# Kernel tuning notes

Hardware: AMD Instinct MI355X
Metric: run time of the kernel (lower is better)

## Reference

```python
import jax, jax.numpy as jnp
import numpy as np


def setup_inputs() -> dict:
    key = jax.random.key(0)
    ks = jax.random.split(key, 7)
    B, D, d1, d2, d3 = 256, 256, 1024, 512, 256
    s = lambda f: 1.0 / np.sqrt(f)  # torch nn.Linear-style init scale
    return {
        "x": jax.random.normal(ks[0], (B, D), jnp.float32),
        "W1": jax.random.normal(ks[1], (d1, D), jnp.float32) * s(D),
        "b1": jax.random.normal(ks[2], (d1,), jnp.float32) * s(D),
        "W2": jax.random.normal(ks[3], (d2, d1), jnp.float32) * s(d1),
        "b2": jax.random.normal(ks[4], (d2,), jnp.float32) * s(d1),
        "W3": jax.random.normal(ks[5], (d3, d2), jnp.float32) * s(d2),
        "b3": jax.random.normal(ks[6], (d3,), jnp.float32) * s(d2),
        "k": 10,
    }


def _border_dists(x, W1, b1, W2, b2, W3, b3):
    # Layer 1: pre-activations and boundary distances. For the first layer the
    # effective linear map is W1 itself (shared across the batch).
    z1 = x @ W1.T + b1                                   # [B, d1]
    dist1 = jnp.abs(z1) / jnp.linalg.norm(W1, axis=1)    # [B, d1]
    m1 = (z1 > 0).astype(x.dtype)
    V1 = m1[:, :, None] * W1[None]                       # [B, d1, D] per-instance map after ReLU
    h1 = m1 * z1

    # Layer 2
    z2 = h1 @ W2.T + b2                                  # [B, d2]
    V2 = jnp.einsum('oi,bid->bod', W2, V1)               # [B, d2, D]
    dist2 = jnp.abs(z2) / jnp.linalg.norm(V2, axis=2)
    m2 = (z2 > 0).astype(x.dtype)
    h2 = m2 * z2

    # Layer 3
    z3 = h2 @ W3.T + b3                                  # [B, d3]
    V3 = jnp.einsum('oi,bid->bod', W3, m2[:, :, None] * V2)  # [B, d3, D]
    dist3 = jnp.abs(z3) / jnp.linalg.norm(V3, axis=2)

    return jnp.concatenate([dist1, dist2, dist3], axis=1)  # [B, d1+d2+d3]


def reference(x, W1, b1, W2, b2, W3, b3, k):
    dists = _border_dists(x, W1, b1, W2, b2, W3, b3)
    # smallest-k distances per instance via top_k on negated distances
    neg_top, _ = jax.lax.top_k(-dists, k)                # [B, k]
    return jnp.sum(-neg_top)                             # border-distance loss (scalar)
```

## Files before the change

kernel.cpp:

```cpp
#include <hip/hip_runtime.h>
#include <math.h>
#include <float.h>

#define B   256
#define D   256
#define D1  1024
#define D2  512
#define D3  256
#define NDIST (D1 + D2 + D3)
#define CQ  2.0f

typedef __attribute__((ext_vector_type(8))) short short8;
typedef __attribute__((ext_vector_type(4))) float f32x4;
typedef __attribute__((ext_vector_type(4))) int   i32x4;

__device__ __forceinline__ float waveReduceSum(float v) {
    #pragma unroll
    for (int off = 32; off > 0; off >>= 1)
        v += __shfl_down(v, off, 64);
    return v;
}
__device__ __forceinline__ float waveReduceMax(float v) {
    #pragma unroll
    for (int off = 32; off > 0; off >>= 1)
        v = fmaxf(v, __shfl_down(v, off, 64));
    return v;
}
__device__ __forceinline__ unsigned short f2bf(float f) {
    unsigned int u = __float_as_uint(f);
    u = (u + 0x7FFFu + ((u >> 16) & 1u)) >> 16;
    return (unsigned short)u;
}
__device__ __forceinline__ float bf2f(unsigned short h) {
    return __uint_as_float(((unsigned int)h) << 16);
}
__device__ __forceinline__ void gld16(const void* g, void* l) {
    __builtin_amdgcn_global_load_lds(
        (const __attribute__((address_space(1))) unsigned int*)g,
        (__attribute__((address_space(3))) unsigned int*)l, 16, 0, 0);
}
__device__ __forceinline__ int swz_src(int row, int lane) {
    return ((lane & 3) + ((row >> 1) & 3)) & 3;
}
__device__ __forceinline__ int swz_frag(int row, int quad) {
    return row * 32 + (((quad - ((row >> 1) & 3)) & 3) * 8);
}

__global__ __launch_bounds__(256) void k_prep(
    const float* __restrict__ x,  const float* __restrict__ W1,
    const float* __restrict__ W2, const float* __restrict__ W3,
    float* __restrict__ zeros,
    float* __restrict__ outp,
    unsigned short* __restrict__ xhi,  unsigned short* __restrict__ xlo,
    unsigned short* __restrict__ W1hi, unsigned short* __restrict__ W1lo,
    unsigned short* __restrict__ W2hi, unsigned short* __restrict__ W2lo,
    unsigned short* __restrict__ W3hi, unsigned short* __restrict__ W3lo,
    signed char* __restrict__ W1Ti8, float* __restrict__ saq,
    signed char* __restrict__ W2i8,  float* __restrict__ sbq,
    signed char* __restrict__ W3i8,  float* __restrict__ s3q,
    float* __restrict__ rn1) {
    int blk = blockIdx.x;
    int t = threadIdx.x;
    if (blk < 1536) {
        if (blk == 0 && t == 0) outp[0] = 0.f;
        zeros[blk * 256 + t] = 0.f;
        return;
    }
    if (blk < 2496) {
        int i4 = ((blk - 1536) * 256 + t) * 4;
        const float* src; unsigned short *hi, *lo; int off;
        if (i4 < 65536)       { src = x;  hi = xhi;  lo = xlo;  off = i4; }
        else if (i4 < 327680) { src = W1; hi = W1hi; lo = W1lo; off = i4 - 65536; }
        else if (i4 < 851968) { src = W2; hi = W2hi; lo = W2lo; off = i4 - 327680; }
        else                  { src = W3; hi = W3hi; lo = W3lo; off = i4 - 851968; }
        float4 v = *(const float4*)(src + off);
        ushort4 h, l;
        h.x = f2bf(v.x); l.x = f2bf(v.x - bf2f(h.x));
        h.y = f2bf(v.y); l.y = f2bf(v.y - bf2f(h.y));
        h.z = f2bf(v.z); l.z = f2bf(v.z - bf2f(h.z));
        h.w = f2bf(v.w); l.w = f2bf(v.w - bf2f(h.w));
        *(ushort4*)(hi + off) = h;
        *(ushort4*)(lo + off) = l;
        return;
    }
    if (blk < 2528) {
        int ty = t >> 5, tx = t & 31;
        int d = (blk - 2496) * 8 + ty;
        float m = 0.f;
        for (int i = tx; i < D1; i += 32) m = fmaxf(m, fabsf(W1[(size_t)i * D + d]));
        #pragma unroll
        for (int off = 16; off > 0; off >>= 1) m = fmaxf(m, __shfl_down(m, off, 32));
        m = __shfl(m, 0, 32);
        m = fmaxf(m, 1e-20f);
        if (tx == 0) saq[d] = m / 127.f;
        float inv = 127.f / m;
        for (int i = tx; i < D1; i += 32) {
            int q = __float2int_rn(W1[(size_t)i * D + d] * inv);
            W1Ti8[(size_t)d * D1 + i] = (signed char)q;
        }
        return;
    }
    if (blk < 2656) {
        int o = (blk - 2528) * 4 + (t >> 6);
        int l = t & 63;
        const float* row = W2 + (size_t)o * D1;
        float m = 0.f;
        for (int tt = l; tt < D1; tt += 64) m = fmaxf(m, fabsf(row[tt]));
        m = waveReduceMax(m);
        m = __shfl(m, 0, 64);
        m = fmaxf(m, 1e-20f);
        if (l == 0) sbq[o] = m / 127.f;
        float inv = 127.f / m;
        for (int tt = l; tt < D1; tt += 64)
            W2i8[(size_t)o * D1 + tt] = (signed char)__float2int_rn(row[tt] * inv);
        return;
    }
    if (blk < 2720) {
        int p = (blk - 2656) * 4 + (t >> 6);
        int l = t & 63;
        const float* row = W3 + (size_t)p * D2;
        float m = 0.f;
        for (int tt = l; tt < D2; tt += 64) m = fmaxf(m, fabsf(row[tt]));
        m = waveReduceMax(m);
        m = __shfl(m, 0, 64);
        m = fmaxf(m, 1e-20f);
        if (l == 0) s3q[p] = m / 127.f;
        float inv = 127.f / m;
        for (int tt = l; tt < D2; tt += 64)
            W3i8[(size_t)p * D2 + tt] = (signed char)__float2int_rn(row[tt] * inv);
        return;
    }
    {
        int gw = (blk - 2720) * 4 + (t >> 6);
        int lane = t & 63;
        const float* row = W1 + (size_t)gw * D;
        float s = 0.f;
        for (int tt = lane; tt < D; tt += 64) { float v = row[tt]; s += v * v; }
        s = waveReduceSum(s);
        if (lane == 0) rn1[gw] = sqrtf(s);
    }
}

template <int KD, int KL>
__device__ __forceinline__ void mfma3_64(
    const unsigned short* __restrict__ Ahi, const unsigned short* __restrict__ Alo,
    const unsigned short* __restrict__ Bhi, const unsigned short* __restrict__ Blo,
    int m0, int n0, int k0, unsigned short* sm, f32x4 acc[2][2]) {
    int tid = threadIdx.x;
    int l = tid & 63, w = tid >> 6;
    int rsub = l >> 2;
    int quad = l >> 4, l16 = l & 15;
    int wm = (w >> 1) * 32, wn = (w & 1) * 32;
    unsigned short* sAh = sm;
    unsigned short* sAl = sm + 2048;
    unsigned short* sBh = sm + 4096;
    unsigned short* sBl = sm + 6144;
    ptrdiff_t dA = Alo - Ahi, dB = Blo - Bhi;
    int rloc = w * 16 + rsub;
    int c = swz_src(rloc, l);
    const unsigned short* pa = Ahi + (size_t)(m0 + rloc) * KD + k0 + c * 8;
    const unsigned short* pb = Bhi + (size_t)(n0 + rloc) * KD + k0 + c * 8;
    int aoff[2], boff[2];
    #pragma unroll
    for (int mt = 0; mt < 2; mt++) aoff[mt] = swz_frag(wm + mt * 16 + l16, quad);
    #pragma unroll
    for (int nt = 0; nt < 2; nt++) boff[nt] = swz_frag(wn + nt * 16 + l16, quad);
    for (int kk = 0; kk < KL; kk += 32) {
        gld16(pa + kk,      sAh + w * 512);
        gld16(pa + dA + kk, sAl + w * 512);
        gld16(pb + kk,      sBh + w * 512);
        gld16(pb + dB + kk, sBl + w * 512);
        __syncthreads();
        short8 ah[2], al[2], bh[2], bl[2];
        #pragma unroll
        for (int mt = 0; mt < 2; mt++) {
            ah[mt] = *(const short8*)(sAh + aoff[mt]);
            al[mt] = *(const short8*)(sAl + aoff[mt]);
        }
        #pragma unroll
        for (int nt = 0; nt < 2; nt++) {
            bh[nt] = *(const short8*)(sBh + boff[nt]);
            bl[nt] = *(const short8*)(sBl + boff[nt]);
        }
        #pragma unroll
        for (int mt = 0; mt < 2; mt++)
            #pragma unroll
            for (int nt = 0; nt < 2; nt++) {
                acc[mt][nt] = __builtin_amdgcn_mfma_f32_16x16x32_bf16(ah[mt], bh[nt], acc[mt][nt], 0, 0, 0);
                acc[mt][nt] = __builtin_amdgcn_mfma_f32_16x16x32_bf16(ah[mt], bl[nt], acc[mt][nt], 0, 0, 0);
                acc[mt][nt] = __builtin_amdgcn_mfma_f32_16x16x32_bf16(al[mt], bh[nt], acc[mt][nt], 0, 0, 0);
            }
        __syncthreads();
    }
}

__global__ __launch_bounds__(256) void k_l1(
    const unsigned short* __restrict__ xhi,  const unsigned short* __restrict__ xlo,
    const unsigned short* __restrict__ W1hi, const unsigned short* __restrict__ W1lo,
    const float* __restrict__ b1, const float* __restrict__ rn1,
    float* __restrict__ dists, unsigned char* __restrict__ m1q,
    unsigned short* __restrict__ h1hi, unsigned short* __restrict__ h1lo) {
    __shared__ __align__(16) unsigned short sm[8192];
    int m0 = blockIdx.x * 64, n0 = blockIdx.y * 64;
    f32x4 acc[2][2] = {};
    mfma3_64<D, D>(xhi, xlo, W1hi, W1lo, m0, n0, 0, sm, acc);
    int l = threadIdx.x & 63, w = threadIdx.x >> 6;
    int quad = l >> 4, l16 = l & 15;
    int wm = (w >> 1) * 32, wn = (w & 1) * 32;
    #pragma unroll
    for (int mt = 0; mt < 2; mt++)
        #pragma unroll
        for (int nt = 0; nt < 2; nt++) {
            int n = n0 + wn + nt * 16 + l16;
            float bv = b1[n], rv = rn1[n];
            #pragma unroll
            for (int r = 0; r < 4; r++) {
                int m = m0 + wm + mt * 16 + quad * 4 + r;
                float z = acc[mt][nt][r] + bv;
                size_t idx = (size_t)m * D1 + n;
                dists[idx] = fabsf(z) / rv;
                m1q[idx] = (z > 0.f) ? 0xFFu : 0u;
                float h = z > 0.f ? z : 0.f;
                unsigned short hh = f2bf(h);
                h1hi[idx] = hh;
                h1lo[idx] = f2bf(h - bf2f(hh));
            }
        }
}

__global__ __launch_bounds__(256) void k_big1(
    const unsigned short* __restrict__ h1hi, const unsigned short* __restrict__ h1lo,
    const unsigned short* __restrict__ W2hi, const unsigned short* __restrict__ W2lo,
    float* __restrict__ z2,
    const signed char* __restrict__ W1Ti8,
    const signed char* __restrict__ W2i8,
    const unsigned char* __restrict__ m1q,
    const float* __restrict__ saq,
    const float* __restrict__ sbq,
    signed char* __restrict__ qV2,
    float* __restrict__ norm2) {
    __shared__ __align__(16) unsigned char smem[32768];
    int bid = blockIdx.x;

    if (bid < 128) {
        unsigned short* sm = (unsigned short*)smem;
        int m0 = (bid & 3) * 64, n0 = ((bid >> 2) & 7) * 64, k0 = (bid >> 5) * 256;
        f32x4 acc[2][2] = {};
        mfma3_64<D1, 256>(h1hi, h1lo, W2hi, W2lo, m0, n0, k0, sm, acc);
        int l = threadIdx.x & 63, w = threadIdx.x >> 6;
        int quad = l >> 4, l16 = l & 15;
        int wm = (w >> 1) * 32, wn = (w & 1) * 32;
        #pragma unroll
        for (int mt = 0; mt < 2; mt++)
            #pragma unroll
            for (int nt = 0; nt < 2; nt++) {
                int n = n0 + wn + nt * 16 + l16;
                #pragma unroll
                for (int r = 0; r < 4; r++) {
                    int m = m0 + wm + mt * 16 + quad * 4 + r;
                    atomicAdd(&z2[(size_t)m * D2 + n], acc[mt][nt][r]);
                }
            }
        return;
    }

    int j = bid - 128;
    signed char* As = (signed char*)smem;
    signed char* Bs = (signed char*)smem + 16384;
    int m0 = (j & 1) * 128;
    int o0 = ((j >> 1) & 3) * 128;
    int bc = j >> 3;
    int b = bc;
    int tid = threadIdx.x;
    int l = tid & 63, w = tid >> 6;
    int quad = l >> 4, l16 = l & 15;
    int wm = (w >> 1) * 64, wn = (w & 1) * 64;
    const unsigned char* mrow = m1q + (size_t)b * D1;

    const signed char* pa[4];
    const signed char* pb[4];
    int lrow = l >> 3, ls = l & 7;
    #pragma unroll
    for (int r = 0; r < 4; r++) {
        int row = r * 32 + w * 8 + lrow;
        int c = (ls + (row & 7)) & 7;
        pa[r] = W1Ti8 + (size_t)(m0 + row) * D1 + c * 16;
        pb[r] = W2i8 + (size_t)(o0 + row) * D1 + c * 16;
    }
    int aoff[4][2], boff[4][2];
    #pragma unroll
    for (int mt = 0; mt < 4; mt++) {
        int tr = wm + mt * 16 + l16;
        #pragma unroll
        for (int ks = 0; ks < 2; ks++)
            aoff[mt][ks] = tr * 128 + (((ks * 4 + quad) - (tr & 7)) & 7) * 16;
    }
    #pragma unroll
    for (int nt = 0; nt < 4; nt++) {
        int tr = wn + nt * 16 + l16;
        #pragma unroll
        for (int ks = 0; ks < 2; ks++)
            boff[nt][ks] = tr * 128 + (((ks * 4 + quad) - (tr & 7)) & 7) * 16;
    }

    i32x4 acc[4][4];
    #pragma unroll
    for (int i = 0; i < 4; i++)
        #pragma unroll
        for (int jj = 0; jj < 4; jj++) acc[i][jj] = (i32x4)0;

    for (int kk = 0; kk < D1; kk += 128) {
        #pragma unroll
        for (int r = 0; r < 4; r++) {
            gld16(pa[r] + kk, As + r * 4096 + w * 1024);
            gld16(pb[r] + kk, Bs + r * 4096 + w * 1024);
        }
        i32x4 mv0 = *(const i32x4*)(mrow + kk + quad * 16);
        i32x4 mv1 = *(const i32x4*)(mrow + kk + 64 + quad * 16);
        __syncthreads();
        #pragma unroll
        for (int ks = 0; ks < 2; ks++) {
            i32x4 mv = ks ? mv1 : mv0;
            i32x4 a[4], bq[4];
            #pragma unroll
            for (int mt = 0; mt < 4; mt++)
                a[mt] = (*(const i32x4*)(As + aoff[mt][ks])) & mv;
            #pragma unroll
            for (int nt = 0; nt < 4; nt++)
                bq[nt] = *(const i32x4*)(Bs + boff[nt][ks]);
            #pragma unroll
            for (int mt = 0; mt < 4; mt++)
                #pragma unroll
                for (int nt = 0; nt < 4; nt++)
                    acc[mt][nt] = __builtin_amdgcn_mfma_i32_16x16x64_i8(
                        a[mt], bq[nt], acc[mt][nt], 0, 0, 0);
        }
        __syncthreads();
    }

    float sad[4][4];
    #pragma unroll
    for (int mt = 0; mt < 4; mt++)
        #pragma unroll
        for (int r = 0; r < 4; r++)
            sad[mt][r] = saq[m0 + wm + mt * 16 + quad * 4 + r];
    float sbv[4], sbdq[4];
    #pragma unroll
    for (int nt = 0; nt < 4; nt++) {
        sbv[nt] = sbq[o0 + wn + nt * 16 + l16];
        sbdq[nt] = sbv[nt] * (1.0f / CQ);
    }

    #pragma unroll
    for (int nt = 0; nt < 4; nt++) {
        float s = 0.f;
        #pragma unroll
        for (int mt = 0; mt < 4; mt++)
            #pragma unroll
            for (int r = 0; r < 4; r++) {
                float v = (float)acc[mt][nt][r] * sad[mt][r] * sbv[nt];
                s += v * v;
            }
        s += __shfl_down(s, 32, 64);
        s += __shfl_down(s, 16, 64);
        if (l < 16)
            atomicAdd(&norm2[(size_t)b * D2 + o0 + wn + nt * 16 + l], s);
    }

    signed char* qb = qV2 + (size_t)bc * (D * D2);
    #pragma unroll
    for (int mt = 0; mt < 4; mt++) {
        int dbase = m0 + wm + mt * 16 + quad * 4;
        #pragma unroll
        for (int r = 0; r < 4; r++)
            #pragma unroll
            for (int nt = 0; nt < 4; nt++) {
                int o = o0 + wn + nt * 16 + l16;
                int qi = __float2int_rn((float)acc[mt][nt][r] * sbdq[nt]);
                qi = max(-127, min(127, qi));
                qb[(size_t)(dbase + r) * D2 + o] = (signed char)qi;
            }
    }
}

__global__ __launch_bounds__(256) void k_l2b(
    const float* __restrict__ b2, float* __restrict__ z2,
    unsigned char* __restrict__ m2q,
    unsigned short* __restrict__ h2hi, unsigned short* __restrict__ h2lo) {
    int idx = blockIdx.x * 256 + threadIdx.x;
    int n = idx & (D2 - 1);
    float z = z2[idx] + b2[n];
    z2[idx] = z;
    m2q[idx] = (z > 0.f) ? 0xFFu : 0u;
    float h = z > 0.f ? z : 0.f;
    unsigned short hh = f2bf(h);
    h2hi[idx] = hh;
    h2lo[idx] = f2bf(h - bf2f(hh));
}

__global__ __launch_bounds__(256) void k_big2(
    const unsigned short* __restrict__ h2hi, const unsigned short* __restrict__ h2lo,
    const unsigned short* __restrict__ W3hi, const unsigned short* __restrict__ W3lo,
    float* __restrict__ z3,
    const signed char* __restrict__ W3i8,
    const signed char* __restrict__ qV2,
    const unsigned char* __restrict__ m2q,
    const float* __restrict__ saq,
    const float* __restrict__ s3q,
    float* __restrict__ norm3) {
    __shared__ __align__(16) unsigned char smem[32768];
    int bid = blockIdx.x;

    if (bid < 32) {
        unsigned short* sm = (unsigned short*)smem;
        int m0 = (bid & 3) * 64, n0 = ((bid >> 2) & 3) * 64, k0 = (bid >> 4) * 256;
        f32x4 acc[2][2] = {};
        mfma3_64<D2, 256>(h2hi, h2lo, W3hi, W3lo, m0, n0, k0, sm, acc);
        int l = threadIdx.x & 63, w = threadIdx.x >> 6;
        int quad = l >> 4, l16 = l & 15;
        int wm = (w >> 1) * 32, wn = (w & 1) * 32;
        #pragma unroll
        for (int mt = 0; mt < 2; mt++)
            #pragma unroll
            for (int nt = 0; nt < 2; nt++) {
                int n = n0 + wn + nt * 16 + l16;
                #pragma unroll
                for (int r = 0; r < 4; r++) {
                    int m = m0 + wm + mt * 16 + quad * 4 + r;
                    atomicAdd(&z3[(size_t)m * D3 + n], acc[mt][nt][r]);
                }
            }
        return;
    }

    int j = bid - 32;
    signed char* As = (signed char*)smem;
    signed char* Bs = (signed char*)smem + 16384;
    int m0 = (j & 1) * 128;
    int n0 = ((j >> 1) & 1) * 128;
    int bc = j >> 2;
    int b = bc;
    int tid = threadIdx.x;
    int l = tid & 63, w = tid >> 6;
    int quad = l >> 4, l16 = l & 15;
    int wm = (w >> 1) * 64, wn = (w & 1) * 64;
    const unsigned char* mrow = m2q + (size_t)b * D2;
    const signed char* Bsrc = qV2 + (size_t)bc * (D * D2);

    const signed char* pa[4];
    const signed char* pb[4];
    int lrow = l >> 3, ls = l & 7;
    #pragma unroll
    for (int r = 0; r < 4; r++) {
        int row = r * 32 + w * 8 + lrow;
        int c = (ls + (row & 7)) & 7;
        pa[r] = W3i8 + (size_t)(m0 + row) * D2 + c * 16;
        pb[r] = Bsrc + (size_t)(n0 + row) * D2 + c * 16;
    }
    int aoff[4][2], boff[4][2];
    #pragma unroll
    for (int mt = 0; mt < 4; mt++) {
        int tr = wm + mt * 16 + l16;
        #pragma unroll
        for (int ks = 0; ks < 2; ks++)
            aoff[mt][ks] = tr * 128 + (((ks * 4 + quad) - (tr & 7)) & 7) * 16;
    }
    #pragma unroll
    for (int nt = 0; nt < 4; nt++) {
        int tr = wn + nt * 16 + l16;
        #pragma unroll
        for (int ks = 0; ks < 2; ks++)
            boff[nt][ks] = tr * 128 + (((ks * 4 + quad) - (tr & 7)) & 7) * 16;
    }

    i32x4 acc[4][4];
    #pragma unroll
    for (int i = 0; i < 4; i++)
        #pragma unroll
        for (int jj = 0; jj < 4; jj++) acc[i][jj] = (i32x4)0;

    for (int kk = 0; kk < D2; kk += 128) {
        #pragma unroll
        for (int r = 0; r < 4; r++) {
            gld16(pa[r] + kk, As + r * 4096 + w * 1024);
            gld16(pb[r] + kk, Bs + r * 4096 + w * 1024);
        }
        i32x4 mv0 = *(const i32x4*)(mrow + kk + quad * 16);
        i32x4 mv1 = *(const i32x4*)(mrow + kk + 64 + quad * 16);
        __syncthreads();
        #pragma unroll
        for (int ks = 0; ks < 2; ks++) {
            i32x4 mv = ks ? mv1 : mv0;
            i32x4 a[4], bq[4];
            #pragma unroll
            for (int mt = 0; mt < 4; mt++)
                a[mt] = *(const i32x4*)(As + aoff[mt][ks]);
            #pragma unroll
            for (int nt = 0; nt < 4; nt++)
                bq[nt] = (*(const i32x4*)(Bs + boff[nt][ks])) & mv;
            #pragma unroll
            for (int mt = 0; mt < 4; mt++)
                #pragma unroll
                for (int nt = 0; nt < 4; nt++)
                    acc[mt][nt] = __builtin_amdgcn_mfma_i32_16x16x64_i8(
                        a[mt], bq[nt], acc[mt][nt], 0, 0, 0);
        }
        __syncthreads();
    }

    float saCQ[4];
    #pragma unroll
    for (int nt = 0; nt < 4; nt++)
        saCQ[nt] = saq[n0 + wn + nt * 16 + l16] * CQ;

    #pragma unroll
    for (int mt = 0; mt < 4; mt++)
        #pragma unroll
        for (int r = 0; r < 4; r++) {
            float s = 0.f;
            #pragma unroll
            for (int nt = 0; nt < 4; nt++) {
                float v = (float)acc[mt][nt][r] * saCQ[nt];
                s += v * v;
            }
            s += __shfl_down(s, 8, 64);
            s += __shfl_down(s, 4, 64);
            s += __shfl_down(s, 2, 64);
            s += __shfl_down(s, 1, 64);
            if (l16 == 0) {
                int p = m0 + wm + mt * 16 + quad * 4 + r;
                float s3 = s3q[p];
                atomicAdd(&norm3[(size_t)b * D3 + p], s * s3 * s3);
            }
        }
}

__global__ __launch_bounds__(256) void k_topk(
    const float* __restrict__ dists,
    const float* __restrict__ z2, const float* __restrict__ norm2,
    const float* __restrict__ z3, const float* __restrict__ b3,
    const float* __restrict__ norm3,
    const int* __restrict__ kp, float* __restrict__ outp) {
    __shared__ unsigned long long wmin[4];
    int b = blockIdx.x, t = threadIdx.x;
    float lv[7];
    #pragma unroll
    for (int j = 0; j < 4; j++) lv[j] = dists[(size_t)b * D1 + t + 256 * j];
    #pragma unroll
    for (int j = 4; j < 6; j++) {
        int o = t + 256 * j - 1024;
        lv[j] = fabsf(z2[(size_t)b * D2 + o]) / sqrtf(norm2[(size_t)b * D2 + o]);
    }
    {
        float zz = z3[(size_t)b * D3 + t] + b3[t];
        lv[6] = fabsf(zz) / sqrtf(norm3[(size_t)b * D3 + t]);
    }
    int k = *kp;
    if (k > NDIST) k = NDIST;
    float sum = 0.f;
    for (int it = 0; it < k; it++) {
        float mv = lv[0]; int mj = 0;
        #pragma unroll
        for (int j = 1; j < 7; j++)
            if (lv[j] < mv) { mv = lv[j]; mj = j; }
        unsigned long long key =
            ((unsigned long long)__float_as_uint(mv) << 32) | (unsigned)(t * 8 + mj);
        #pragma unroll
        for (int off = 32; off > 0; off >>= 1) {
            unsigned long long o = __shfl_down(key, off, 64);
            if (o < key) key = o;
        }
        if ((t & 63) == 0) wmin[t >> 6] = key;
        __syncthreads();
        unsigned long long k0 = wmin[0];
        #pragma unroll
        for (int ww = 1; ww < 4; ww++) if (wmin[ww] < k0) k0 = wmin[ww];
        sum += __uint_as_float((unsigned)(k0 >> 32));
        int wt = (int)((k0 & 0xFFFu) >> 3), wj = (int)(k0 & 7u);
        if (t == wt) lv[wj] = FLT_MAX;
        __syncthreads();
    }
    if (t == 0) atomicAdd(outp, sum);
}

extern "C" void kernel_launch(void* const* d_in, const int* in_sizes, int n_in,
                              void* d_out, int out_size, void* d_ws, size_t ws_size,
                              hipStream_t stream) {
    const float* x  = (const float*)d_in[0];
    const float* W1 = (const float*)d_in[1];
    const float* b1 = (const float*)d_in[2];
    const float* W2 = (const float*)d_in[3];
    const float* b2 = (const float*)d_in[4];
    const float* W3 = (const float*)d_in[5];
    const float* b3 = (const float*)d_in[6];
    const int*   kp = (const int*)d_in[7];
    float* outp = (float*)d_out;

    float* fp = (float*)d_ws;
    float* rn1     = fp;                          fp += D1;
    float* dists   = fp;                          fp += (size_t)B * D1;
    float* saq     = fp;                          fp += D;
    float* sbq     = fp;                          fp += D2;
    float* s3q     = fp;                          fp += D3;
    float* z2      = fp;                          fp += (size_t)B * D2;
    float* z3      = fp;                          fp += (size_t)B * D3;
    float* norm2   = fp;                          fp += (size_t)B * D2;
    float* norm3   = fp;                          fp += (size_t)B * D3;
    unsigned short* up = (unsigned short*)fp;
    unsigned short* W2hi  = up;  up += (size_t)D2 * D1;
    unsigned short* W2lo  = up;  up += (size_t)D2 * D1;
    unsigned short* W3hi  = up;  up += (size_t)D3 * D2;
    unsigned short* W3lo  = up;  up += (size_t)D3 * D2;
    unsigned short* xhi   = up;  up += (size_t)B * D;
    unsigned short* xlo   = up;  up += (size_t)B * D;
    unsigned short* W1hi  = up;  up += (size_t)D1 * D;
    unsigned short* W1lo  = up;  up += (size_t)D1 * D;
    unsigned short* h1hi  = up;  up += (size_t)B * D1;
    unsigned short* h1lo  = up;  up += (size_t)B * D1;
    unsigned short* h2hi  = up;  up += (size_t)B * D2;
    unsigned short* h2lo  = up;  up += (size_t)B * D2;
    signed char*    cp = (signed char*)up;
    signed char*    W1Ti8 = cp;  cp += (size_t)D * D1;
    signed char*    W2i8  = cp;  cp += (size_t)D2 * D1;
    signed char*    W3i8  = cp;  cp += (size_t)D3 * D2;
    unsigned char*  m1q   = (unsigned char*)cp;  cp += (size_t)B * D1;
    unsigned char*  m2q   = (unsigned char*)cp;  cp += (size_t)B * D2;
    signed char*    qV2   = cp;

    k_prep<<<2976, 256, 0, stream>>>(x, W1, W2, W3, z2, outp,
                                     xhi, xlo, W1hi, W1lo, W2hi, W2lo, W3hi, W3lo,
                                     W1Ti8, saq, W2i8, sbq, W3i8, s3q, rn1);

    k_l1<<<dim3(B / 64, D1 / 64), 256, 0, stream>>>(xhi, xlo, W1hi, W1lo, b1, rn1,
                                                    dists, m1q, h1hi, h1lo);

    k_big1<<<2176, 256, 0, stream>>>(h1hi, h1lo, W2hi, W2lo, z2,
                                     W1Ti8, W2i8, m1q, saq, sbq, qV2, norm2);

    k_l2b<<<(B * D2) / 256, 256, 0, stream>>>(b2, z2, m2q, h2hi, h2lo);

    k_big2<<<1056, 256, 0, stream>>>(h2hi, h2lo, W3hi, W3lo, z3,
                                     W3i8, qV2, m2q, saq, s3q, norm3);

    k_topk<<<B, 256, 0, stream>>>(dists, z2, norm2, z3, b3, norm3, kp, outp);
}
```

Measured before the change: 180.7 us.

## Process two batch rows per block in big1 and full D per block in big2

In k_big1 each block now computes the V2 tile for two batch instances at once. It reuses the same W1T/W2 int8 tiles loaded into shared memory and applies each instance's mask in registers, which halves the grid. In k_big2 each block now covers both 128-wide D halves, loading two B tiles against a single A tile, which halves the A loads and the grid. The cost is doubled accumulator registers (32 i32x4 per thread), which may cut occupancy, and more shared memory in k_big2 (48KB).

```diff
diff --git a/kernel.cpp b/kernel.cpp
--- a/kernel.cpp
+++ b/kernel.cpp
@@ -269,13 +269,13 @@
     signed char* Bs = (signed char*)smem + 16384;
     int m0 = (j & 1) * 128;
     int o0 = ((j >> 1) & 3) * 128;
-    int bc = j >> 3;
-    int b = bc;
+    int bp = j >> 3;
     int tid = threadIdx.x;
     int l = tid & 63, w = tid >> 6;
     int quad = l >> 4, l16 = l & 15;
     int wm = (w >> 1) * 64, wn = (w & 1) * 64;
-    const unsigned char* mrow = m1q + (size_t)b * D1;
+    const unsigned char* mrow0 = m1q + (size_t)(bp * 2) * D1;
+    const unsigned char* mrow1 = m1q + (size_t)(bp * 2 + 1) * D1;
 
     const signed char* pa[4];
     const signed char* pb[4];
@@ -303,11 +303,13 @@
             boff[nt][ks] = tr * 128 + (((ks * 4 + quad) - (tr & 7)) & 7) * 16;
     }
 
-    i32x4 acc[4][4];
-    #pragma unroll
-    for (int i = 0; i < 4; i++)
-        #pragma unroll
-        for (int jj = 0; jj < 4; jj++) acc[i][jj] = (i32x4)0;
+    i32x4 acc[2][4][4];
+    #pragma unroll
+    for (int bb = 0; bb < 2; bb++)
+        #pragma unroll
+        for (int i = 0; i < 4; i++)
+            #pragma unroll
+            for (int jj = 0; jj < 4; jj++) acc[bb][i][jj] = (i32x4)0;
 
     for (int kk = 0; kk < D1; kk += 128) {
         #pragma unroll
@@ -315,25 +317,38 @@
             gld16(pa[r] + kk, As + r * 4096 + w * 1024);
             gld16(pb[r] + kk, Bs + r * 4096 + w * 1024);
         }
-        i32x4 mv0 = *(const i32x4*)(mrow + kk + quad * 16);
-        i32x4 mv1 = *(const i32x4*)(mrow + kk + 64 + quad * 16);
+        i32x4 mA0 = *(const i32x4*)(mrow0 + kk + quad * 16);
+        i32x4 mA1 = *(const i32x4*)(mrow0 + kk + 64 + quad * 16);
+        i32x4 mB0 = *(const i32x4*)(mrow1 + kk + quad * 16);
+        i32x4 mB1 = *(const i32x4*)(mrow1 + kk + 64 + quad * 16);
         __syncthreads();
         #pragma unroll
         for (int ks = 0; ks < 2; ks++) {
-            i32x4 mv = ks ? mv1 : mv0;
-            i32x4 a[4], bq[4];
+            i32x4 araw[4], bq[4];
             #pragma unroll
             for (int mt = 0; mt < 4; mt++)
-                a[mt] = (*(const i32x4*)(As + aoff[mt][ks])) & mv;
+                araw[mt] = *(const i32x4*)(As + aoff[mt][ks]);
             #pragma unroll
             for (int nt = 0; nt < 4; nt++)
                 bq[nt] = *(const i32x4*)(Bs + boff[nt][ks]);
-            #pragma unroll
-            for (int mt = 0; mt < 4; mt++)
+            i32x4 mv0 = ks ? mA1 : mA0;
+            i32x4 mv1 = ks ? mB1 : mB0;
+            #pragma unroll
+            for (int mt = 0; mt < 4; mt++) {
+                i32x4 a0 = araw[mt] & mv0;
                 #pragma unroll
                 for (int nt = 0; nt < 4; nt++)
-                    acc[mt][nt] = __builtin_amdgcn_mfma_i32_16x16x64_i8(
-                        a[mt], bq[nt], acc[mt][nt], 0, 0, 0);
+                    acc[0][mt][nt] = __builtin_amdgcn_mfma_i32_16x16x64_i8(
+                        a0, bq[nt], acc[0][mt][nt], 0, 0, 0);
+            }
+            #pragma unroll
+            for (int mt = 0; mt < 4; mt++) {
+                i32x4 a1 = araw[mt] & mv1;
+                #pragma unroll
+                for (int nt = 0; nt < 4; nt++)
+                    acc[1][mt][nt] = __builtin_amdgcn_mfma_i32_16x16x64_i8(
+                        a1, bq[nt], acc[1][mt][nt], 0, 0, 0);
+            }
         }
         __syncthreads();
     }
@@ -352,34 +367,37 @@
     }
 
     #pragma unroll
-    for (int nt = 0; nt < 4; nt++) {
-        float s = 0.f;
-        #pragma unroll
-        for (int mt = 0; mt < 4; mt++)
-            #pragma unroll
-            for (int r = 0; r < 4; r++) {
-                float v = (float)acc[mt][nt][r] * sad[mt][r] * sbv[nt];
-                s += v * v;
-            }
-        s += __shfl_down(s, 32, 64);
-        s += __shfl_down(s, 16, 64);
-        if (l < 16)
-            atomicAdd(&norm2[(size_t)b * D2 + o0 + wn + nt * 16 + l], s);
-    }
-
-    signed char* qb = qV2 + (size_t)bc * (D * D2);
-    #pragma unroll
-    for (int mt = 0; mt < 4; mt++) {
-        int dbase = m0 + wm + mt * 16 + quad * 4;
-        #pragma unroll
-        for (int r = 0; r < 4; r++)
-            #pragma unroll
-            for (int nt = 0; nt < 4; nt++) {
-                int o = o0 + wn + nt * 16 + l16;
-                int qi = __float2int_rn((float)acc[mt][nt][r] * sbdq[nt]);
-                qi = max(-127, min(127, qi));
-                qb[(size_t)(dbase + r) * D2 + o] = (signed char)qi;
-            }
+    for (int bb = 0; bb < 2; bb++) {
+        int b = bp * 2 + bb;
+        #pragma unroll
+        for (int nt = 0; nt < 4; nt++) {
+            float s = 0.f;
+            #pragma unroll
+            for (int mt = 0; mt < 4; mt++)
+                #pragma unroll
+                for (int r = 0; r < 4; r++) {
+                    float v = (float)acc[bb][mt][nt][r] * sad[mt][r] * sbv[nt];
+                    s += v * v;
+                }
+            s += __shfl_down(s, 32, 64);
+            s += __shfl_down(s, 16, 64);
+            if (l < 16)
+                atomicAdd(&norm2[(size_t)b * D2 + o0 + wn + nt * 16 + l], s);
+        }
+        signed char* qb = qV2 + (size_t)b * (D * D2);
+        #pragma unroll
+        for (int mt = 0; mt < 4; mt++) {
+            int dbase = m0 + wm + mt * 16 + quad * 4;
+            #pragma unroll
+            for (int r = 0; r < 4; r++)
+                #pragma unroll
+                for (int nt = 0; nt < 4; nt++) {
+                    int o = o0 + wn + nt * 16 + l16;
+                    int qi = __float2int_rn((float)acc[bb][mt][nt][r] * sbdq[nt]);
+                    qi = max(-127, min(127, qi));
+                    qb[(size_t)(dbase + r) * D2 + o] = (signed char)qi;
+                }
+        }
     }
 }
 
@@ -408,7 +426,7 @@
     const float* __restrict__ saq,
     const float* __restrict__ s3q,
     float* __restrict__ norm3) {
-    __shared__ __align__(16) unsigned char smem[32768];
+    __shared__ __align__(16) unsigned char smem[49152];
     int bid = blockIdx.x;
 
     if (bid < 32) {
@@ -434,28 +452,29 @@
     }
 
     int j = bid - 32;
-    signed char* As = (signed char*)smem;
-    signed char* Bs = (signed char*)smem + 16384;
+    signed char* As  = (signed char*)smem;
+    signed char* Bs0 = (signed char*)smem + 16384;
+    signed char* Bs1 = (signed char*)smem + 32768;
     int m0 = (j & 1) * 128;
-    int n0 = ((j >> 1) & 1) * 128;
-    int bc = j >> 2;
-    int b = bc;
+    int bc = j >> 1;
     int tid = threadIdx.x;
     int l = tid & 63, w = tid >> 6;
     int quad = l >> 4, l16 = l & 15;
     int wm = (w >> 1) * 64, wn = (w & 1) * 64;
-    const unsigned char* mrow = m2q + (size_t)b * D2;
+    const unsigned char* mrow = m2q + (size_t)bc * D2;
     const signed char* Bsrc = qV2 + (size_t)bc * (D * D2);
 
     const signed char* pa[4];
-    const signed char* pb[4];
+    const signed char* pb0[4];
+    const signed char* pb1[4];
     int lrow = l >> 3, ls = l & 7;
     #pragma unroll
     for (int r = 0; r < 4; r++) {
         int row = r * 32 + w * 8 + lrow;
         int c = (ls + (row & 7)) & 7;
-        pa[r] = W3i8 + (size_t)(m0 + row) * D2 + c * 16;
-        pb[r] = Bsrc + (size_t)(n0 + row) * D2 + c * 16;
+        pa[r]  = W3i8 + (size_t)(m0 + row) * D2 + c * 16;
+        pb0[r] = Bsrc + (size_t)row * D2 + c * 16;
+        pb1[r] = Bsrc + (size_t)(128 + row) * D2 + c * 16;
     }
     int aoff[4][2], boff[4][2];
     #pragma unroll
@@ -473,17 +492,20 @@
             boff[nt][ks] = tr * 128 + (((ks * 4 + quad) - (tr & 7)) & 7) * 16;
     }
 
-    i32x4 acc[4][4];
-    #pragma unroll
-    for (int i = 0; i < 4; i++)
-        #pragma unroll
-        for (int jj = 0; jj < 4; jj++) acc[i][jj] = (i32x4)0;
+    i32x4 acc[2][4][4];
+    #pragma unroll
+    for (int dd = 0; dd < 2; dd++)
+        #pragma unroll
+        for (int i = 0; i < 4; i++)
+            #pragma unroll
+            for (int jj = 0; jj < 4; jj++) acc[dd][i][jj] = (i32x4)0;
 
     for (int kk = 0; kk < D2; kk += 128) {
         #pragma unroll
         for (int r = 0; r < 4; r++) {
-            gld16(pa[r] + kk, As + r * 4096 + w * 1024);
-            gld16(pb[r] + kk, Bs + r * 4096 + w * 1024);
+            gld16(pa[r] + kk,  As  + r * 4096 + w * 1024);
+            gld16(pb0[r] + kk, Bs0 + r * 4096 + w * 1024);
+            gld16(pb1[r] + kk, Bs1 + r * 4096 + w * 1024);
         }
         i32x4 mv0 = *(const i32x4*)(mrow + kk + quad * 16);
         i32x4 mv1 = *(const i32x4*)(mrow + kk + 64 + quad * 16);
@@ -491,27 +513,36 @@
         #pragma unroll
         for (int ks = 0; ks < 2; ks++) {
             i32x4 mv = ks ? mv1 : mv0;
-            i32x4 a[4], bq[4];
+            i32x4 a[4];
             #pragma unroll
             for (int mt = 0; mt < 4; mt++)
                 a[mt] = *(const i32x4*)(As + aoff[mt][ks]);
             #pragma unroll
-            for (int nt = 0; nt < 4; nt++)
-                bq[nt] = (*(const i32x4*)(Bs + boff[nt][ks])) & mv;
-            #pragma unroll
-            for (int mt = 0; mt < 4; mt++)
-                #pragma unroll
-                for (int nt = 0; nt < 4; nt++)
-                    acc[mt][nt] = __builtin_amdgcn_mfma_i32_16x16x64_i8(
-                        a[mt], bq[nt], acc[mt][nt], 0, 0, 0);
-        }
-        __syncthreads();
-    }
-
-    float saCQ[4];
-    #pragma unroll
-    for (int nt = 0; nt < 4; nt++)
-        saCQ[nt] = saq[n0 + wn + nt * 16 + l16] * CQ;
+            for (int nt = 0; nt < 4; nt++) {
+                i32x4 b0 = (*(const i32x4*)(Bs0 + boff[nt][ks])) & mv;
+                #pragma unroll
+                for (int mt = 0; mt < 4; mt++)
+                    acc[0][mt][nt] = __builtin_amdgcn_mfma_i32_16x16x64_i8(
+                        a[mt], b0, acc[0][mt][nt], 0, 0, 0);
+            }
+            #pragma unroll
+            for (int nt = 0; nt < 4; nt++) {
+                i32x4 b1 = (*(const i32x4*)(Bs1 + boff[nt][ks])) & mv;
+                #pragma unroll
+                for (int mt = 0; mt < 4; mt++)
+                    acc[1][mt][nt] = __builtin_amdgcn_mfma_i32_16x16x64_i8(
+                        a[mt], b1, acc[1][mt][nt], 0, 0, 0);
+            }
+        }
+        __syncthreads();
+    }
+
+    float saCQ0[4], saCQ1[4];
+    #pragma unroll
+    for (int nt = 0; nt < 4; nt++) {
+        saCQ0[nt] = saq[wn + nt * 16 + l16] * CQ;
+        saCQ1[nt] = saq[128 + wn + nt * 16 + l16] * CQ;
+    }
 
     #pragma unroll
     for (int mt = 0; mt < 4; mt++)
@@ -520,8 +551,9 @@
             float s = 0.f;
             #pragma unroll
             for (int nt = 0; nt < 4; nt++) {
-                float v = (float)acc[mt][nt][r] * saCQ[nt];
-                s += v * v;
+                float v0 = (float)acc[0][mt][nt][r] * saCQ0[nt];
+                float v1 = (float)acc[1][mt][nt][r] * saCQ1[nt];
+                s += v0 * v0 + v1 * v1;
             }
             s += __shfl_down(s, 8, 64);
             s += __shfl_down(s, 4, 64);
@@ -530,7 +562,7 @@
             if (l16 == 0) {
                 int p = m0 + wm + mt * 16 + quad * 4 + r;
                 float s3 = s3q[p];
-                atomicAdd(&norm3[(size_t)b * D3 + p], s * s3 * s3);
+                atomicAdd(&norm3[(size_t)bc * D3 + p], s * s3 * s3);
             }
         }
 }
@@ -634,13 +666,13 @@
     k_l1<<<dim3(B / 64, D1 / 64), 256, 0, stream>>>(xhi, xlo, W1hi, W1lo, b1, rn1,
                                                     dists, m1q, h1hi, h1lo);
 
-    k_big1<<<2176, 256, 0, stream>>>(h1hi, h1lo, W2hi, W2lo, z2,
+    k_big1<<<1152, 256, 0, stream>>>(h1hi, h1lo, W2hi, W2lo, z2,
                                      W1Ti8, W2i8, m1q, saq, sbq, qV2, norm2);
 
     k_l2b<<<(B * D2) / 256, 256, 0, stream>>>(b2, z2, m2q, h2hi, h2lo);
 
-    k_big2<<<1056, 256, 0, stream>>>(h2hi, h2lo, W3hi, W3lo, z3,
-                                     W3i8, qV2, m2q, saq, s3q, norm3);
+    k_big2<<<544, 256, 0, stream>>>(h2hi, h2lo, W3hi, W3lo, z3,
+                                    W3i8, qV2, m2q, saq, s3q, norm3);
 
     k_topk<<<B, 256, 0, stream>>>(dists, z2, norm2, z3, b3, norm3, kp, outp);
 }
```

Result: slower. 195.1 us (+8.0%).

## Fuse layer-2 bias/ReLU into layer-3 kernel and coalesce qV2 stores via LDS

Applied to the files above, without the earlier changes.

Removes the separate k_l2b kernel. Its bias add, ReLU mask and bf16 hi/lo split are now computed inside k_big2: the GEMM blocks build h2 tiles on the fly from z2+b2, and the int8 blocks rebuild the mask row into shared memory. k_topk adds b2 itself. Separately, k_big1 stages its quantized V2 tile in padded shared memory and writes it with 16-byte coalesced stores instead of scattered byte stores. This saves a launch and intermediate global traffic, at the cost of redundant mask and conversion work across blocks and an extra barrier.

```diff
diff --git a/kernel.cpp b/kernel.cpp
--- a/kernel.cpp
+++ b/kernel.cpp
@@ -269,8 +269,7 @@
     signed char* Bs = (signed char*)smem + 16384;
     int m0 = (j & 1) * 128;
     int o0 = ((j >> 1) & 3) * 128;
-    int bc = j >> 3;
-    int b = bc;
+    int b = j >> 3;
     int tid = threadIdx.x;
     int l = tid & 63, w = tid >> 6;
     int quad = l >> 4, l16 = l & 15;
@@ -367,58 +366,108 @@
             atomicAdd(&norm2[(size_t)b * D2 + o0 + wn + nt * 16 + l], s);
     }
 
-    signed char* qb = qV2 + (size_t)bc * (D * D2);
+    unsigned char* qt = (unsigned char*)smem;
     #pragma unroll
     for (int mt = 0; mt < 4; mt++) {
-        int dbase = m0 + wm + mt * 16 + quad * 4;
+        int dl = wm + mt * 16 + quad * 4;
         #pragma unroll
         for (int r = 0; r < 4; r++)
             #pragma unroll
             for (int nt = 0; nt < 4; nt++) {
-                int o = o0 + wn + nt * 16 + l16;
+                int ol = wn + nt * 16 + l16;
                 int qi = __float2int_rn((float)acc[mt][nt][r] * sbdq[nt]);
                 qi = max(-127, min(127, qi));
-                qb[(size_t)(dbase + r) * D2 + o] = (signed char)qi;
-            }
-    }
-}
-
-__global__ __launch_bounds__(256) void k_l2b(
-    const float* __restrict__ b2, float* __restrict__ z2,
-    unsigned char* __restrict__ m2q,
-    unsigned short* __restrict__ h2hi, unsigned short* __restrict__ h2lo) {
-    int idx = blockIdx.x * 256 + threadIdx.x;
-    int n = idx & (D2 - 1);
-    float z = z2[idx] + b2[n];
-    z2[idx] = z;
-    m2q[idx] = (z > 0.f) ? 0xFFu : 0u;
-    float h = z > 0.f ? z : 0.f;
-    unsigned short hh = f2bf(h);
-    h2hi[idx] = hh;
-    h2lo[idx] = f2bf(h - bf2f(hh));
+                qt[(dl + r) * 144 + ol] = (unsigned char)(signed char)qi;
+            }
+    }
+    __syncthreads();
+    signed char* qb = qV2 + (size_t)b * (D * D2);
+    int row = tid >> 1, half = tid & 1;
+    const unsigned char* srcp = qt + row * 144 + half * 64;
+    signed char* dstp = qb + (size_t)(m0 + row) * D2 + o0 + half * 64;
+    #pragma unroll
+    for (int jj = 0; jj < 4; jj++)
+        *(uint4*)(dstp + jj * 16) = *(const uint4*)(srcp + jj * 16);
 }
 
 __global__ __launch_bounds__(256) void k_big2(
-    const unsigned short* __restrict__ h2hi, const unsigned short* __restrict__ h2lo,
+    const float* __restrict__ z2,
+    const float* __restrict__ b2,
     const unsigned short* __restrict__ W3hi, const unsigned short* __restrict__ W3lo,
     float* __restrict__ z3,
     const signed char* __restrict__ W3i8,
     const signed char* __restrict__ qV2,
-    const unsigned char* __restrict__ m2q,
     const float* __restrict__ saq,
     const float* __restrict__ s3q,
     float* __restrict__ norm3) {
-    __shared__ __align__(16) unsigned char smem[32768];
+    __shared__ __align__(16) unsigned char smem[33280];
     int bid = blockIdx.x;
+    int tid = threadIdx.x;
 
     if (bid < 32) {
-        unsigned short* sm = (unsigned short*)smem;
+        unsigned short* sAh = (unsigned short*)smem;
+        unsigned short* sAl = sAh + 2048;
+        unsigned short* sBh = sAh + 4096;
+        unsigned short* sBl = sAh + 6144;
         int m0 = (bid & 3) * 64, n0 = ((bid >> 2) & 3) * 64, k0 = (bid >> 4) * 256;
-        f32x4 acc[2][2] = {};
-        mfma3_64<D2, 256>(h2hi, h2lo, W3hi, W3lo, m0, n0, k0, sm, acc);
-        int l = threadIdx.x & 63, w = threadIdx.x >> 6;
+        int l = tid & 63, w = tid >> 6;
+        int rsub = l >> 2;
         int quad = l >> 4, l16 = l & 15;
         int wm = (w >> 1) * 32, wn = (w & 1) * 32;
+        int rloc = w * 16 + rsub;
+        int c = swz_src(rloc, l);
+        const float* pz  = z2 + (size_t)(m0 + rloc) * D2 + k0 + c * 8;
+        const float* pbi = b2 + k0 + c * 8;
+        const unsigned short* pb = W3hi + (size_t)(n0 + rloc) * D2 + k0 + c * 8;
+        ptrdiff_t dB = W3lo - W3hi;
+        int aoff[2], boff[2];
+        #pragma unroll
+        for (int mt = 0; mt < 2; mt++) aoff[mt] = swz_frag(wm + mt * 16 + l16, quad);
+        #pragma unroll
+        for (int nt = 0; nt < 2; nt++) boff[nt] = swz_frag(wn + nt * 16 + l16, quad);
+        int wrA = w * 512 + l * 8;
+        f32x4 acc[2][2] = {};
+        for (int kk = 0; kk < 256; kk += 32) {
+            gld16(pb + kk,      sBh + w * 512);
+            gld16(pb + dB + kk, sBl + w * 512);
+            float4 za = *(const float4*)(pz + kk);
+            float4 zb = *(const float4*)(pz + kk + 4);
+            float4 ba = *(const float4*)(pbi + kk);
+            float4 bb = *(const float4*)(pbi + kk + 4);
+            float hv[8] = { za.x + ba.x, za.y + ba.y, za.z + ba.z, za.w + ba.w,
+                            zb.x + bb.x, zb.y + bb.y, zb.z + bb.z, zb.w + bb.w };
+            short8 h8, l8;
+            #pragma unroll
+            for (int q2 = 0; q2 < 8; q2++) {
+                float h = hv[q2] > 0.f ? hv[q2] : 0.f;
+                unsigned short hh = f2bf(h);
+                h8[q2] = (short)hh;
+                l8[q2] = (short)f2bf(h - bf2f(hh));
+            }
+            *(short8*)(sAh + wrA) = h8;
+            *(short8*)(sAl + wrA) = l8;
+            __syncthreads();
+            short8 ah[2], al[2], bh[2], bl[2];
+            #pragma unroll
+            for (int mt = 0; mt < 2; mt++) {
+                ah[mt] = *(const short8*)(sAh + aoff[mt]);
+                al[mt] = *(const short8*)(sAl + aoff[mt]);
+            }
+            #pragma unroll
+            for (int nt = 0; nt < 2; nt++) {
+                bh[nt] = *(const short8*)(sBh + boff[nt]);
+                bl[nt] = *(const short8*)(sBl + boff[nt]);
+            }
+            #pragma unroll
+            for (int mt = 0; mt < 2; mt++)
+                #pragma unroll
+                for (int nt = 0; nt < 2; nt++) {
+                    acc[mt][nt] = __builtin_amdgcn_mfma_f32_16x16x32_bf16(ah[mt], bh[nt], acc[mt][nt], 0, 0, 0);
+                    acc[mt][nt] = __builtin_amdgcn_mfma_f32_16x16x32_bf16(ah[mt], bl[nt], acc[mt][nt], 0, 0, 0);
+                    acc[mt][nt] = __builtin_amdgcn_mfma_f32_16x16x32_bf16(al[mt], bh[nt], acc[mt][nt], 0, 0, 0);
+                }
+            __syncthreads();
+        }
         #pragma unroll
         for (int mt = 0; mt < 2; mt++)
             #pragma unroll
@@ -436,16 +485,24 @@
     int j = bid - 32;
     signed char* As = (signed char*)smem;
     signed char* Bs = (signed char*)smem + 16384;
+    unsigned char* mbuf = (unsigned char*)smem + 32768;
     int m0 = (j & 1) * 128;
     int n0 = ((j >> 1) & 1) * 128;
     int bc = j >> 2;
-    int b = bc;
-    int tid = threadIdx.x;
     int l = tid & 63, w = tid >> 6;
     int quad = l >> 4, l16 = l & 15;
     int wm = (w >> 1) * 64, wn = (w & 1) * 64;
-    const unsigned char* mrow = m2q + (size_t)b * D2;
     const signed char* Bsrc = qV2 + (size_t)bc * (D * D2);
+
+    {
+        #pragma unroll
+        for (int rr = 0; rr < 2; rr++) {
+            int o = tid * 2 + rr;
+            float z = z2[(size_t)bc * D2 + o] + b2[o];
+            mbuf[o] = (z > 0.f) ? 0xFFu : 0u;
+        }
+    }
+    __syncthreads();
 
     const signed char* pa[4];
     const signed char* pb[4];
@@ -485,9 +542,9 @@
             gld16(pa[r] + kk, As + r * 4096 + w * 1024);
             gld16(pb[r] + kk, Bs + r * 4096 + w * 1024);
         }
-        i32x4 mv0 = *(const i32x4*)(mrow + kk + quad * 16);
-        i32x4 mv1 = *(const i32x4*)(mrow + kk + 64 + quad * 16);
         __syncthreads();
+        i32x4 mv0 = *(const i32x4*)(mbuf + kk + quad * 16);
+        i32x4 mv1 = *(const i32x4*)(mbuf + kk + 64 + quad * 16);
         #pragma unroll
         for (int ks = 0; ks < 2; ks++) {
             i32x4 mv = ks ? mv1 : mv0;
@@ -530,14 +587,15 @@
             if (l16 == 0) {
                 int p = m0 + wm + mt * 16 + quad * 4 + r;
                 float s3 = s3q[p];
-                atomicAdd(&norm3[(size_t)b * D3 + p], s * s3 * s3);
+                atomicAdd(&norm3[(size_t)bc * D3 + p], s * s3 * s3);
             }
         }
 }
 
 __global__ __launch_bounds__(256) void k_topk(
     const float* __restrict__ dists,
-    const float* __restrict__ z2, const float* __restrict__ norm2,
+    const float* __restrict__ z2, const float* __restrict__ b2,
+    const float* __restrict__ norm2,
     const float* __restrict__ z3, const float* __restrict__ b3,
     const float* __restrict__ norm3,
     const int* __restrict__ kp, float* __restrict__ outp) {
@@ -549,7 +607,8 @@
     #pragma unroll
     for (int j = 4; j < 6; j++) {
         int o = t + 256 * j - 1024;
-        lv[j] = fabsf(z2[(size_t)b * D2 + o]) / sqrtf(norm2[(size_t)b * D2 + o]);
+        float zz = z2[(size_t)b * D2 + o] + b2[o];
+        lv[j] = fabsf(zz) / sqrtf(norm2[(size_t)b * D2 + o]);
     }
     {
         float zz = z3[(size_t)b * D3 + t] + b3[t];
@@ -617,14 +676,11 @@
     unsigned short* W1lo  = up;  up += (size_t)D1 * D;
     unsigned short* h1hi  = up;  up += (size_t)B * D1;
     unsigned short* h1lo  = up;  up += (size_t)B * D1;
-    unsigned short* h2hi  = up;  up += (size_t)B * D2;
-    unsigned short* h2lo  = up;  up += (size_t)B * D2;
     signed char*    cp = (signed char*)up;
     signed char*    W1Ti8 = cp;  cp += (size_t)D * D1;
     signed char*    W2i8  = cp;  cp += (size_t)D2 * D1;
     signed char*    W3i8  = cp;  cp += (size_t)D3 * D2;
     unsigned char*  m1q   = (unsigned char*)cp;  cp += (size_t)B * D1;
-    unsigned char*  m2q   = (unsigned char*)cp;  cp += (size_t)B * D2;
     signed char*    qV2   = cp;
 
     k_prep<<<2976, 256, 0, stream>>>(x, W1, W2, W3, z2, outp,
@@ -637,10 +693,8 @@
     k_big1<<<2176, 256, 0, stream>>>(h1hi, h1lo, W2hi, W2lo, z2,
                                      W1Ti8, W2i8, m1q, saq, sbq, qV2, norm2);
 
-    k_l2b<<<(B * D2) / 256, 256, 0, stream>>>(b2, z2, m2q, h2hi, h2lo);
-
-    k_big2<<<1056, 256, 0, stream>>>(h2hi, h2lo, W3hi, W3lo, z3,
-                                     W3i8, qV2, m2q, saq, s3q, norm3);
-
-    k_topk<<<B, 256, 0, stream>>>(dists, z2, norm2, z3, b3, norm3, kp, outp);
-}
+    k_big2<<<1056, 256, 0, stream>>>(z2, b2, W3hi, W3lo, z3,
+                                     W3i8, qV2, saq, s3q, norm3);
+
+    k_topk<<<B, 256, 0, stream>>>(dists, z2, b2, norm2, z3, b3, norm3, kp, outp);
+}
```

Result: no change. 181.2 us (+0.3%).
